# Performance work log

Hardware: AMD Instinct MI355X
Metric: run time of the kernel (lower is better)

Reference implementation:

```python
import jax, jax.numpy as jnp
import numpy as np

B, T, C = 4, 2048, 2048  # batch, n_target, n_context
KEY_SIZE = 1024
VALUE_SIZE = 1024
NUM_HEADS = 16
KEY_HIDDEN = 64
HEAD_SIZE = VALUE_SIZE // NUM_HEADS  # 64
NORMALISE = True


def setup_inputs() -> dict:
    key = jax.random.key(0)
    ks = jax.random.split(key, 7)
    s = 0.02
    return {
        "queries": jax.random.normal(ks[0], (B, T, KEY_SIZE), jnp.float32),
        "keys": jax.random.normal(ks[1], (B, C, KEY_SIZE), jnp.float32),
        "values": jax.random.normal(ks[2], (B, C, VALUE_SIZE), jnp.float32),
        "Wq": jax.random.normal(ks[3], (NUM_HEADS * KEY_HIDDEN, KEY_SIZE), jnp.float32) * s,
        "Wk": jax.random.normal(ks[4], (NUM_HEADS * KEY_HIDDEN, KEY_SIZE), jnp.float32) * s,
        "Wv": jax.random.normal(ks[5], (NUM_HEADS * HEAD_SIZE, VALUE_SIZE), jnp.float32) * s,
        "Wo": jax.random.normal(ks[6], (VALUE_SIZE, NUM_HEADS * HEAD_SIZE), jnp.float32) * s,
    }


def reference(queries, keys, values, Wq, Wk, Wv, Wo):
    # Linear projections (torch nn.Linear: x @ W.T), reshape to heads
    q = (queries @ Wq.T).reshape(B, T, NUM_HEADS, KEY_HIDDEN)   # [B,T,H,Dk]
    k = (keys @ Wk.T).reshape(B, C, NUM_HEADS, KEY_HIDDEN)      # [B,C,H,Dk]
    v = (values @ Wv.T).reshape(B, C, NUM_HEADS, HEAD_SIZE)     # [B,C,H,Dv]
    scale = np.sqrt(KEY_HIDDEN).astype(np.float32)
    # Scores [B,H,T,C]
    scores = jnp.einsum('bthd,bchd->bhtc', q, k) / scale
    if NORMALISE:
        attn = jax.nn.softmax(scores, axis=-1)
    else:
        attn = jax.nn.sigmoid(scores)
    out = jnp.einsum('bhtc,bchd->bthd', attn, v)                # [B,T,H,Dv]
    out = out.reshape(B, T, NUM_HEADS * HEAD_SIZE)
    return out @ Wo.T                                            # [B,T,VALUE_SIZE]
```

## Files before the change

kernel.cpp:

```cpp
#include <hip/hip_runtime.h>
#include <stdint.h>

#define BATCH 4
#define SEQ   2048
#define EMB   1024
#define NH    16
#define HD    64

typedef __attribute__((ext_vector_type(4))) float  floatx4;
typedef __attribute__((ext_vector_type(8))) short  shortx8;

__device__ __forceinline__ unsigned short f2bf(float f) {
  unsigned u = __builtin_bit_cast(unsigned, f);
  u += 0x7FFFu + ((u >> 16) & 1u);
  return (unsigned short)(u >> 16);
}

__device__ __forceinline__ unsigned pack2bf(float a, float b) {
  return (unsigned)f2bf(a) | ((unsigned)f2bf(b) << 16);
}

__device__ __forceinline__ unsigned packtrunc(float a, float b) {
#if __has_builtin(__builtin_amdgcn_perm)
  return __builtin_amdgcn_perm(__builtin_bit_cast(unsigned, b),
                               __builtin_bit_cast(unsigned, a), 0x07060302u);
#else
  return (__builtin_bit_cast(unsigned, a) >> 16) |
         (__builtin_bit_cast(unsigned, b) & 0xFFFF0000u);
#endif
}

__device__ __forceinline__ float fexp2(float x) {
#if __has_builtin(__builtin_amdgcn_exp2f)
  return __builtin_amdgcn_exp2f(x);
#else
  return exp2f(x);
#endif
}

__device__ __forceinline__ void gl_lds16(const void* g, void* l) {
  __builtin_amdgcn_global_load_lds((const __attribute__((address_space(1))) void*)g,
                                   (__attribute__((address_space(3))) void*)l,
                                   16, 0, 0);
}

__device__ __forceinline__ void cast_body(const float* __restrict__ in,
                                          unsigned short* __restrict__ out, int bb, int t) {
  size_t i = (size_t)bb * 256 + t;
  const float4* p = (const float4*)in + i * 2;
  float4 f0 = p[0], f1 = p[1];
  uint4 o;
  o.x = pack2bf(f0.x, f0.y);
  o.y = pack2bf(f0.z, f0.w);
  o.z = pack2bf(f1.x, f1.y);
  o.w = pack2bf(f1.z, f1.w);
  ((uint4*)out)[i] = o;
}

__global__ __launch_bounds__(256) void cast_bf16(const float* __restrict__ in,
                                                 unsigned short* __restrict__ out) {
  cast_body(in, out, blockIdx.x, threadIdx.x);
}

__global__ __launch_bounds__(256) void cast_all(
    const float* __restrict__ q, const float* __restrict__ k, const float* __restrict__ v,
    const float* __restrict__ w0, const float* __restrict__ w1,
    const float* __restrict__ w2, const float* __restrict__ w3,
    unsigned short* __restrict__ oq, unsigned short* __restrict__ ok, unsigned short* __restrict__ ov,
    unsigned short* __restrict__ ow0, unsigned short* __restrict__ ow1,
    unsigned short* __restrict__ ow2, unsigned short* __restrict__ ow3) {
  int bb = blockIdx.x;
  const float* in; unsigned short* out;
  if      (bb < 4096)  { in = q;  out = oq; }
  else if (bb < 8192)  { in = k;  out = ok;  bb -= 4096; }
  else if (bb < 12288) { in = v;  out = ov;  bb -= 8192; }
  else if (bb < 12800) { in = w0; out = ow0; bb -= 12288; }
  else if (bb < 13312) { in = w1; out = ow1; bb -= 12800; }
  else if (bb < 13824) { in = w2; out = ow2; bb -= 13312; }
  else                 { in = w3; out = ow3; bb -= 13824; }
  cast_body(in, out, bb, threadIdx.x);
}

__global__ __launch_bounds__(256) void cast_w4(const float* __restrict__ i0, const float* __restrict__ i1,
                                               const float* __restrict__ i2, const float* __restrict__ i3,
                                               unsigned short* __restrict__ o0, unsigned short* __restrict__ o1,
                                               unsigned short* __restrict__ o2, unsigned short* __restrict__ o3) {
  int bb = blockIdx.x;
  const float* in; unsigned short* out;
  if      (bb < 512)  { in = i0; out = o0; }
  else if (bb < 1024) { in = i1; out = o1; bb -= 512; }
  else if (bb < 1536) { in = i2; out = o2; bb -= 1024; }
  else                { in = i3; out = o3; bb -= 1536; }
  cast_body(in, out, bb, threadIdx.x);
}

#define TST 136
template <int MODE>
__device__ __forceinline__ void gemm_body(const unsigned short* __restrict__ A,
                                          const unsigned short* __restrict__ Bt,
                                          void* __restrict__ Cp, float cscale,
                                          unsigned short* As, unsigned short* Bs,
                                          unsigned short* Ts) {
  constexpr int N = EMB, K = EMB;
  constexpr int BM = 128, BN = 128, BK = 64;
  const int t = threadIdx.x, w = t >> 6, lane = t & 63;
  const int quad = lane >> 4, lrow = lane & 15;
  const int m0 = blockIdx.y * BM, n0 = blockIdx.x * BN;
  const int wm = (w >> 1) * 64, wn = (w & 1) * 64;
  floatx4 acc[4][4] = {};

  const unsigned short* asrc[4];
  const unsigned short* bsrc[4];
#pragma unroll
  for (int i = 0; i < 4; i++) {
    int q = i * 256 + t;
    int r = q >> 3, kc = (q & 7) ^ (r & 7);
    asrc[i] = A + (size_t)(m0 + r) * K + kc * 8;
    bsrc[i] = Bt + (size_t)(n0 + r) * K + kc * 8;
  }

  for (int k0 = 0; k0 < K; k0 += BK) {
#pragma unroll
    for (int i = 0; i < 4; i++) {
      gl_lds16(asrc[i], (char*)As + (size_t)(i * 256 + w * 64) * 16);
      gl_lds16(bsrc[i], (char*)Bs + (size_t)(i * 256 + w * 64) * 16);
      asrc[i] += BK; bsrc[i] += BK;
    }
    __syncthreads();
#pragma unroll
    for (int ks = 0; ks < 2; ks++) {
      shortx8 a[4];
#pragma unroll
      for (int mi = 0; mi < 4; mi++) {
        int row = wm + mi * 16 + lrow;
        a[mi] = *(const shortx8*)(As + row * 64 + (((ks * 4 + quad) ^ (row & 7)) * 8));
      }
#pragma unroll
      for (int ni = 0; ni < 4; ni++) {
        int rowb = wn + ni * 16 + lrow;
        shortx8 b = *(const shortx8*)(Bs + rowb * 64 + (((ks * 4 + quad) ^ (rowb & 7)) * 8));
#pragma unroll
        for (int mi = 0; mi < 4; mi++)
          acc[mi][ni] = __builtin_amdgcn_mfma_f32_16x16x32_bf16(a[mi], b, acc[mi][ni], 0, 0, 0);
      }
    }
    __syncthreads();
  }

  if constexpr (MODE == 2) {
#pragma unroll
    for (int u = 0; u < 2; u++)
#pragma unroll
      for (int ni = 0; ni < 4; ni++) {
        uint4 p;
        p.x = pack2bf(acc[2 * u][ni][0], acc[2 * u + 1][ni][0]);
        p.y = pack2bf(acc[2 * u][ni][1], acc[2 * u + 1][ni][1]);
        p.z = pack2bf(acc[2 * u][ni][2], acc[2 * u + 1][ni][2]);
        p.w = pack2bf(acc[2 * u][ni][3], acc[2 * u + 1][ni][3]);
        int col = wn + ni * 16 + lrow;
        int cloc = wm + u * 32 + quad * 8;
        *(uint4*)(Ts + col * TST + cloc) = p;
      }
    __syncthreads();
    unsigned short* vTout = (unsigned short*)Cp;
    const int b = m0 >> 11, cbase = m0 & 2047, h0 = n0 >> 6;
#pragma unroll
    for (int i = 0; i < 8; i++) {
      int g = t + 256 * i;
      int hh2 = g >> 10, d = (g >> 4) & 63, a = g & 15;
      uint4 v = *(const uint4*)(Ts + (hh2 * 64 + d) * TST + a * 8);
      *(uint4*)(vTout + ((size_t)((b * NH + h0 + hh2) * HD + d)) * SEQ + cbase + a * 8) = v;
    }
    __syncthreads();
  } else {
#pragma unroll
    for (int mi = 0; mi < 4; mi++)
#pragma unroll
      for (int ni = 0; ni < 4; ni++)
#pragma unroll
        for (int r = 0; r < 4; r++) {
          int row = m0 + wm + mi * 16 + quad * 4 + r;
          int col = n0 + wn + ni * 16 + lrow;
          float v = acc[mi][ni][r] * cscale;
          if constexpr (MODE == 1) ((float*)Cp)[(size_t)row * N + col] = v;
          else                     ((unsigned short*)Cp)[(size_t)row * N + col] = f2bf(v);
        }
  }
}

__global__ __launch_bounds__(256, 2) void gemm_qkv(
    const unsigned short* __restrict__ Xq, const unsigned short* __restrict__ Xk,
    const unsigned short* __restrict__ Xv,
    const unsigned short* __restrict__ Wq, const unsigned short* __restrict__ Wk,
    const unsigned short* __restrict__ Wv,
    unsigned short* __restrict__ Oq, unsigned short* __restrict__ Ok,
    unsigned short* __restrict__ OvT, float sq) {
  __shared__ unsigned short As[128 * 64];
  __shared__ unsigned short Bs[128 * 64];
  __shared__ unsigned short Ts[128 * TST];
  if (blockIdx.z == 0)      gemm_body<0>(Xq, Wq, Oq, sq,   As, Bs, Ts);
  else if (blockIdx.z == 1) gemm_body<0>(Xk, Wk, Ok, 1.0f, As, Bs, Ts);
  else                      gemm_body<2>(Xv, Wv, OvT, 1.0f, As, Bs, Ts);
}

__global__ __launch_bounds__(256, 2) void gemm_b(const unsigned short* __restrict__ A,
                                                 const unsigned short* __restrict__ Bt,
                                                 unsigned short* __restrict__ C, float sc) {
  __shared__ unsigned short As[128 * 64];
  __shared__ unsigned short Bs[128 * 64];
  gemm_body<0>(A, Bt, C, sc, As, Bs, nullptr);
}
__global__ __launch_bounds__(256, 2) void gemm_vt(const unsigned short* __restrict__ A,
                                                  const unsigned short* __restrict__ Bt,
                                                  unsigned short* __restrict__ C) {
  __shared__ unsigned short As[128 * 64];
  __shared__ unsigned short Bs[128 * 64];
  __shared__ unsigned short Ts[128 * TST];
  gemm_body<2>(A, Bt, C, 1.0f, As, Bs, Ts);
}
__global__ __launch_bounds__(256, 2) void gemm_o(const unsigned short* __restrict__ A,
                                                 const unsigned short* __restrict__ Bt,
                                                 float* __restrict__ C) {
  __shared__ unsigned short As[128 * 64];
  __shared__ unsigned short Bs[128 * 64];
  gemm_body<1>(A, Bt, C, 1.0f, As, Bs, nullptr);
}

__global__ __launch_bounds__(256, 4) void flash_attn(const unsigned short* __restrict__ qp,
                                                     const unsigned short* __restrict__ kp,
                                                     const unsigned short* __restrict__ vT,
                                                     unsigned short* __restrict__ ao) {
  __shared__ unsigned short Ks[64 * 64];
  __shared__ unsigned short Vts[64 * 64];
  __shared__ unsigned short Ps[4][16 * 40];
  const int h = blockIdx.x & (NH - 1), b = blockIdx.x >> 4;
  const int t0 = blockIdx.y * 128;
  const int t = threadIdx.x, w = t >> 6, lane = t & 63;
  const int quad = lane >> 4, lrow = lane & 15;

  shortx8 qfrag[2][2];
#pragma unroll
  for (int kk = 0; kk < 2; kk++)
#pragma unroll
    for (int mi = 0; mi < 2; mi++) {
      int row = w * 32 + mi * 16 + lrow;
      qfrag[kk][mi] = *(const shortx8*)(qp + ((size_t)(b * SEQ + t0 + row)) * EMB +
                                        h * HD + kk * 32 + quad * 8);
    }

  const unsigned short* ksrc[2];
  const unsigned short* vsrc[2];
#pragma unroll
  for (int i = 0; i < 2; i++) {
    int p = i * 256 + t;
    int r = p >> 3, kc = (p & 7) ^ (r & 7);
    ksrc[i] = kp + ((size_t)(b * SEQ + r)) * EMB + h * HD + kc * 8;
    vsrc[i] = vT + ((size_t)((b * NH + h) * HD + r)) * SEQ + kc * 8;
  }

  float l_st[2][4] = {};
  floatx4 accO[2][4] = {};

  for (int c0 = 0; c0 < SEQ; c0 += 64) {
    __syncthreads();
#pragma unroll
    for (int i = 0; i < 2; i++) {
      gl_lds16(ksrc[i], (char*)Ks + (size_t)(i * 256 + w * 64) * 16);
      gl_lds16(vsrc[i], (char*)Vts + (size_t)(i * 256 + w * 64) * 16);
      ksrc[i] += 64 * EMB;
      vsrc[i] += 64;
    }
    __syncthreads();

    floatx4 accS[2][4] = {};
#pragma unroll
    for (int kk = 0; kk < 2; kk++) {
      int qk = quad + kk * 4;
#pragma unroll
      for (int ni = 0; ni < 4; ni++) {
        int rowb = ni * 16 + lrow;
        shortx8 bfr = *(const shortx8*)(Ks + rowb * 64 + ((qk ^ (rowb & 7)) * 8));
#pragma unroll
        for (int mi = 0; mi < 2; mi++)
          accS[mi][ni] = __builtin_amdgcn_mfma_f32_16x16x32_bf16(qfrag[kk][mi], bfr, accS[mi][ni], 0, 0, 0);
      }
    }

#pragma unroll
    for (int hh = 0; hh < 2; hh++) {
      shortx8 pafr[2];
#pragma unroll
      for (int mi = 0; mi < 2; mi++) {
#pragma unroll
        for (int r = 0; r < 4; r++) {
          float p0 = fexp2(accS[mi][2 * hh][r]);
          float p1 = fexp2(accS[mi][2 * hh + 1][r]);
          l_st[mi][r] += p0 + p1;
          *(unsigned*)(&Ps[w][(quad * 4 + r) * 40 + lrow * 2]) = packtrunc(p0, p1);
        }
        pafr[mi] = *(const shortx8*)(&Ps[w][lrow * 40 + quad * 8]);
      }
#pragma unroll
      for (int nio = 0; nio < 4; nio++) {
        int d = nio * 16 + lrow;
        shortx8 bfr = *(const shortx8*)(Vts + d * 64 + ((((hh << 2) + quad) ^ (d & 7)) * 8));
#pragma unroll
        for (int mi = 0; mi < 2; mi++)
          accO[mi][nio] = __builtin_amdgcn_mfma_f32_16x16x32_bf16(pafr[mi], bfr, accO[mi][nio], 0, 0, 0);
      }
    }
  }

#pragma unroll
  for (int mi = 0; mi < 2; mi++)
#pragma unroll
    for (int r = 0; r < 4; r++) {
      float l = l_st[mi][r];
      l += __shfl_xor(l, 1);
      l += __shfl_xor(l, 2);
      l += __shfl_xor(l, 4);
      l += __shfl_xor(l, 8);
      float inv = 1.0f / l;
#pragma unroll
      for (int nio = 0; nio < 4; nio++) accO[mi][nio][r] *= inv;
    }
#pragma unroll
  for (int mi = 0; mi < 2; mi++)
#pragma unroll
    for (int nio = 0; nio < 4; nio++)
#pragma unroll
      for (int r = 0; r < 4; r++) {
        int row = t0 + w * 32 + mi * 16 + quad * 4 + r;
        int col = h * HD + nio * 16 + lrow;
        ao[((size_t)(b * SEQ + row)) * EMB + col] = f2bf(accO[mi][nio][r]);
      }
}

extern "C" void kernel_launch(void* const* d_in, const int* in_sizes, int n_in,
                              void* d_out, int out_size, void* d_ws, size_t ws_size,
                              hipStream_t stream) {
  const float* queries = (const float*)d_in[0];
  const float* keys    = (const float*)d_in[1];
  const float* values  = (const float*)d_in[2];
  const float* Wq      = (const float*)d_in[3];
  const float* Wk      = (const float*)d_in[4];
  const float* Wv      = (const float*)d_in[5];
  const float* Wo      = (const float*)d_in[6];

  char* ws = (char*)d_ws;
  const size_t MB = 1ull << 20;
  const float SC2 = 0.125f * 1.44269504088896341f;

  unsigned short* wq_b = (unsigned short*)(ws + 0 * MB);
  unsigned short* wk_b = (unsigned short*)(ws + 2 * MB);
  unsigned short* wv_b = (unsigned short*)(ws + 4 * MB);
  unsigned short* wo_b = (unsigned short*)(ws + 6 * MB);

  dim3 gg(EMB / 128, (BATCH * SEQ) / 128);
  dim3 fg(NH * BATCH, SEQ / 128);

  if (ws_size >= 104 * MB) {
    unsigned short* Xq = (unsigned short*)(ws + 8 * MB);
    unsigned short* Xk = (unsigned short*)(ws + 24 * MB);
    unsigned short* Xv = (unsigned short*)(ws + 40 * MB);
    unsigned short* qp = (unsigned short*)(ws + 56 * MB);
    unsigned short* kp = (unsigned short*)(ws + 72 * MB);
    unsigned short* vT = (unsigned short*)(ws + 88 * MB);
    unsigned short* ao = Xq;

    cast_all<<<14336, 256, 0, stream>>>(queries, keys, values, Wq, Wk, Wv, Wo,
                                        Xq, Xk, Xv, wq_b, wk_b, wv_b, wo_b);
    gemm_qkv<<<dim3(gg.x, gg.y, 3), 256, 0, stream>>>(Xq, Xk, Xv, wq_b, wk_b, wv_b,
                                                      qp, kp, vT, SC2);
    flash_attn<<<fg, 256, 0, stream>>>(qp, kp, vT, ao);
    gemm_o<<<gg, 256, 0, stream>>>(ao, wo_b, (float*)d_out);
  } else {
    unsigned short* X  = (unsigned short*)(ws + 8 * MB);
    unsigned short* qp = (unsigned short*)(ws + 24 * MB);
    unsigned short* kp = (unsigned short*)(ws + 40 * MB);
    unsigned short* vT = (unsigned short*)(ws + 56 * MB);
    unsigned short* ao = X;

    cast_w4<<<2048, 256, 0, stream>>>(Wq, Wk, Wv, Wo, wq_b, wk_b, wv_b, wo_b);
    cast_bf16<<<4096, 256, 0, stream>>>(queries, X);
    gemm_b<<<gg, 256, 0, stream>>>(X, wq_b, qp, SC2);
    cast_bf16<<<4096, 256, 0, stream>>>(keys, X);
    gemm_b<<<gg, 256, 0, stream>>>(X, wk_b, kp, 1.0f);
    cast_bf16<<<4096, 256, 0, stream>>>(values, X);
    gemm_vt<<<gg, 256, 0, stream>>>(X, wv_b, vT);
    flash_attn<<<fg, 256, 0, stream>>>(qp, kp, vT, ao);
    gemm_o<<<gg, 256, 0, stream>>>(ao, wo_b, (float*)d_out);
  }
}
```

Baseline: 321.0 us.

## Double-buffer K/V tiles in flash attention and split QKV projection launch

The flash attention loop now keeps two LDS buffers for K and V tiles and prefetches the next tile while computing on the current one. This replaces the two barriers per iteration with one and overlaps the global loads with MFMA work. It also raises wave priority around the MFMA sections. Separately, the fused QKV GEMM is split into a Q/K kernel without the transpose scratch LDS and a separate V-transpose GEMM, so the Q/K blocks use less shared memory. The cost is doubled K/V LDS in attention, which may lower occupancy, plus one extra kernel launch.

```diff
diff --git a/kernel.cpp b/kernel.cpp
--- a/kernel.cpp
+++ b/kernel.cpp
@@ -188,19 +188,14 @@
   }
 }
 
-__global__ __launch_bounds__(256, 2) void gemm_qkv(
+__global__ __launch_bounds__(256, 2) void gemm_qk(
     const unsigned short* __restrict__ Xq, const unsigned short* __restrict__ Xk,
-    const unsigned short* __restrict__ Xv,
     const unsigned short* __restrict__ Wq, const unsigned short* __restrict__ Wk,
-    const unsigned short* __restrict__ Wv,
-    unsigned short* __restrict__ Oq, unsigned short* __restrict__ Ok,
-    unsigned short* __restrict__ OvT, float sq) {
+    unsigned short* __restrict__ Oq, unsigned short* __restrict__ Ok, float sq) {
   __shared__ unsigned short As[128 * 64];
   __shared__ unsigned short Bs[128 * 64];
-  __shared__ unsigned short Ts[128 * TST];
-  if (blockIdx.z == 0)      gemm_body<0>(Xq, Wq, Oq, sq,   As, Bs, Ts);
-  else if (blockIdx.z == 1) gemm_body<0>(Xk, Wk, Ok, 1.0f, As, Bs, Ts);
-  else                      gemm_body<2>(Xv, Wv, OvT, 1.0f, As, Bs, Ts);
+  if (blockIdx.z == 0) gemm_body<0>(Xq, Wq, Oq, sq,   As, Bs, nullptr);
+  else                 gemm_body<0>(Xk, Wk, Ok, 1.0f, As, Bs, nullptr);
 }
 
 __global__ __launch_bounds__(256, 2) void gemm_b(const unsigned short* __restrict__ A,
@@ -230,8 +225,8 @@
                                                      const unsigned short* __restrict__ kp,
                                                      const unsigned short* __restrict__ vT,
                                                      unsigned short* __restrict__ ao) {
-  __shared__ unsigned short Ks[64 * 64];
-  __shared__ unsigned short Vts[64 * 64];
+  __shared__ unsigned short Ks[2][64 * 64];
+  __shared__ unsigned short Vts[2][64 * 64];
   __shared__ unsigned short Ps[4][16 * 40];
   const int h = blockIdx.x & (NH - 1), b = blockIdx.x >> 4;
   const int t0 = blockIdx.y * 128;
@@ -261,30 +256,45 @@
   float l_st[2][4] = {};
   floatx4 accO[2][4] = {};
 
+#pragma unroll
+  for (int i = 0; i < 2; i++) {
+    gl_lds16(ksrc[i], (char*)Ks[0] + (size_t)(i * 256 + w * 64) * 16);
+    gl_lds16(vsrc[i], (char*)Vts[0] + (size_t)(i * 256 + w * 64) * 16);
+    ksrc[i] += 64 * EMB;
+    vsrc[i] += 64;
+  }
+  __syncthreads();
+
   for (int c0 = 0; c0 < SEQ; c0 += 64) {
-    __syncthreads();
-#pragma unroll
-    for (int i = 0; i < 2; i++) {
-      gl_lds16(ksrc[i], (char*)Ks + (size_t)(i * 256 + w * 64) * 16);
-      gl_lds16(vsrc[i], (char*)Vts + (size_t)(i * 256 + w * 64) * 16);
-      ksrc[i] += 64 * EMB;
-      vsrc[i] += 64;
-    }
-    __syncthreads();
+    const int cur = (c0 >> 6) & 1;
+    const unsigned short* Kc = Ks[cur];
+    const unsigned short* Vc = Vts[cur];
+
+    if (c0 + 64 < SEQ) {
+#pragma unroll
+      for (int i = 0; i < 2; i++) {
+        gl_lds16(ksrc[i], (char*)Ks[cur ^ 1] + (size_t)(i * 256 + w * 64) * 16);
+        gl_lds16(vsrc[i], (char*)Vts[cur ^ 1] + (size_t)(i * 256 + w * 64) * 16);
+        ksrc[i] += 64 * EMB;
+        vsrc[i] += 64;
+      }
+    }
 
     floatx4 accS[2][4] = {};
+    __builtin_amdgcn_s_setprio(1);
 #pragma unroll
     for (int kk = 0; kk < 2; kk++) {
       int qk = quad + kk * 4;
 #pragma unroll
       for (int ni = 0; ni < 4; ni++) {
         int rowb = ni * 16 + lrow;
-        shortx8 bfr = *(const shortx8*)(Ks + rowb * 64 + ((qk ^ (rowb & 7)) * 8));
+        shortx8 bfr = *(const shortx8*)(Kc + rowb * 64 + ((qk ^ (rowb & 7)) * 8));
 #pragma unroll
         for (int mi = 0; mi < 2; mi++)
           accS[mi][ni] = __builtin_amdgcn_mfma_f32_16x16x32_bf16(qfrag[kk][mi], bfr, accS[mi][ni], 0, 0, 0);
       }
     }
+    __builtin_amdgcn_s_setprio(0);
 
 #pragma unroll
     for (int hh = 0; hh < 2; hh++) {
@@ -300,15 +310,19 @@
         }
         pafr[mi] = *(const shortx8*)(&Ps[w][lrow * 40 + quad * 8]);
       }
+      __builtin_amdgcn_s_setprio(1);
 #pragma unroll
       for (int nio = 0; nio < 4; nio++) {
         int d = nio * 16 + lrow;
-        shortx8 bfr = *(const shortx8*)(Vts + d * 64 + ((((hh << 2) + quad) ^ (d & 7)) * 8));
+        shortx8 bfr = *(const shortx8*)(Vc + d * 64 + ((((hh << 2) + quad) ^ (d & 7)) * 8));
 #pragma unroll
         for (int mi = 0; mi < 2; mi++)
           accO[mi][nio] = __builtin_amdgcn_mfma_f32_16x16x32_bf16(pafr[mi], bfr, accO[mi][nio], 0, 0, 0);
       }
-    }
+      __builtin_amdgcn_s_setprio(0);
+    }
+
+    __syncthreads();
   }
 
 #pragma unroll
@@ -370,8 +384,8 @@
 
     cast_all<<<14336, 256, 0, stream>>>(queries, keys, values, Wq, Wk, Wv, Wo,
                                         Xq, Xk, Xv, wq_b, wk_b, wv_b, wo_b);
-    gemm_qkv<<<dim3(gg.x, gg.y, 3), 256, 0, stream>>>(Xq, Xk, Xv, wq_b, wk_b, wv_b,
-                                                      qp, kp, vT, SC2);
+    gemm_qk<<<dim3(gg.x, gg.y, 2), 256, 0, stream>>>(Xq, Xk, wq_b, wk_b, qp, kp, SC2);
+    gemm_vt<<<gg, 256, 0, stream>>>(Xv, wv_b, vT);
     flash_attn<<<fg, 256, 0, stream>>>(qp, kp, vT, ao);
     gemm_o<<<gg, 256, 0, stream>>>(ao, wo_b, (float*)d_out);
   } else {
```

Result: no change. 325.0 us (+1.3%).
